# Optimization experiments

Measured on AMD Instinct MI355X. Metric: run time of the kernel, lower is better.

## Reference

```python
import jax, jax.numpy as jnp
import numpy as np

N_GROUP = 8
TOPK_GROUP = 4
TOP_K = 8
ROUTED_SCALING_FACTOR = 2.5


def setup_inputs() -> dict:
    key = jax.random.key(0)
    ks = jax.random.split(key, 6)
    T, H, I, E = 256, 1024, 512, 32
    x = jax.random.normal(ks[0], (T, H), dtype=jnp.float32)
    gate_w = jax.random.normal(ks[1], (H, E), dtype=jnp.float32) * 0.05
    e_score_bias = jax.random.normal(ks[2], (E,), dtype=jnp.float32) * 0.05
    Wg = jax.random.normal(ks[3], (E, H, I), dtype=jnp.float32) * 0.02
    Wu = jax.random.normal(ks[4], (E, H, I), dtype=jnp.float32) * 0.02
    Wd = jax.random.normal(ks[5], (E, I, H), dtype=jnp.float32) * 0.02
    return {"x": x, "gate_w": gate_w, "e_score_bias": e_score_bias,
            "Wg": Wg, "Wu": Wu, "Wd": Wd}


def _route_ds3(x, gate_w, e_score_bias):
    # DeepSeek-V3 group-limited top-k routing (routing_ds3 in source).
    T = x.shape[0]
    E = gate_w.shape[1]
    logits = x @ gate_w                      # [T, E]
    scores = jax.nn.sigmoid(logits)
    scores_for_choice = scores + e_score_bias[None, :]
    gsz = E // N_GROUP
    grouped = scores_for_choice.reshape(T, N_GROUP, gsz)
    # group score = sum of top-2 expert scores in group
    group_scores = jnp.sum(jax.lax.top_k(grouped, 2)[0], axis=-1)     # [T, n_group]
    _, group_idx = jax.lax.top_k(group_scores, TOPK_GROUP)            # [T, topk_group]
    rows = jnp.arange(T)[:, None]
    group_mask = jnp.zeros((T, N_GROUP), scores.dtype).at[rows, group_idx].set(1.0)
    score_mask = jnp.repeat(group_mask, gsz, axis=-1)                 # [T, E]
    masked = jnp.where(score_mask > 0, scores_for_choice, 0.0)
    _, topk_idx = jax.lax.top_k(masked, TOP_K)                        # [T, k]
    topk_w = jnp.take_along_axis(scores, topk_idx, axis=1)            # gather raw scores
    topk_w = topk_w / (jnp.sum(topk_w, axis=-1, keepdims=True) + 1e-20)
    topk_w = topk_w * ROUTED_SCALING_FACTOR
    return topk_idx, topk_w


def reference(x, gate_w, e_score_bias, Wg, Wu, Wd):
    T = x.shape[0]
    E = gate_w.shape[1]
    topk_idx, topk_w = _route_ds3(x, gate_w, e_score_bias)
    # dense [T, E] routing-weight matrix (topk indices are unique per row)
    rows = jnp.arange(T)[:, None]
    rw = jnp.zeros((T, E), x.dtype).at[rows, topk_idx].set(topk_w)
    # expert gated MLP (silu), combined with routing weights
    g = jnp.einsum('th,ehi->tei', x, Wg)      # [T, E, I]
    u = jnp.einsum('th,ehi->tei', x, Wu)
    a = jax.nn.silu(g) * u
    y = jnp.einsum('tei,eih->teh', a, Wd)     # [T, E, H]
    out = jnp.einsum('te,teh->th', rw, y)     # weighted combine
    return out
```

## Files before the change

kernel.cpp:

```cpp
#include <hip/hip_runtime.h>
#include <cstdint>
#include <cmath>

constexpr int TT   = 256;
constexpr int HD   = 1024;
constexpr int IDIM = 512;
constexpr int NE   = 32;
constexpr int NGRP = 8;
constexpr int TKG  = 4;
constexpr int TOPK = 8;
constexpr float RSCALE = 2.5f;

constexpr int NSX  = HD / 32;
constexpr int NSA  = IDIM / 32;
constexpr int SLAB = 16 * 64 * 8;

typedef float    f32x4 __attribute__((ext_vector_type(4)));
typedef _Float16 half8 __attribute__((ext_vector_type(8)));

constexpr size_t WS_CNT = 0;
constexpr size_t WS_TOK = 256;
constexpr size_t WS_WL  = WS_TOK + (size_t)NE * TT * 4;
constexpr size_t WS_XE  = WS_WL  + (size_t)NE * TT * 4;
constexpr size_t WS_A   = WS_XE  + (size_t)NE * NSX * SLAB * 2;

#define GLOAD16(GP, LP) __builtin_amdgcn_global_load_lds(                      \
    (const __attribute__((address_space(1))) unsigned int*)(GP),               \
    (__attribute__((address_space(3))) unsigned int*)(LP), 16, 0, 0)

__global__ __launch_bounds__(256) void k_route(
    const float* __restrict__ x, const float* __restrict__ gw,
    const float* __restrict__ bias, int* __restrict__ cnt,
    int* __restrict__ tok, float* __restrict__ wl)
{
    int t = blockIdx.x;
    int tid = threadIdx.x;
    int e2 = (tid & 15) * 2;
    int c  = tid >> 4;
    const float* xr = x + (size_t)t * HD;

    float a0 = 0.f, a1 = 0.f;
    int h0 = c * (HD / 16);
#pragma unroll 8
    for (int h = h0; h < h0 + HD / 16; ++h) {
        float xv = xr[h];
        float2 wv = *(const float2*)&gw[(size_t)h * NE + e2];
        a0 += xv * wv.x;
        a1 += xv * wv.y;
    }

    __shared__ float part[16][NE];
    part[c][e2]     = a0;
    part[c][e2 + 1] = a1;
    __syncthreads();

    __shared__ float sc[NE], sfc[NE];
    if (tid < NE) {
        float s = 0.f;
#pragma unroll
        for (int cc = 0; cc < 16; ++cc) s += part[cc][tid];
        float sig = 1.f / (1.f + expf(-s));
        sc[tid]  = sig;
        sfc[tid] = sig + bias[tid];
    }
    __syncthreads();

    if (tid == 0) {
        float gs[NGRP];
        for (int g = 0; g < NGRP; ++g) {
            float m1 = -3.0e38f, m2 = -3.0e38f;
            for (int j = 0; j < 4; ++j) {
                float v = sfc[4 * g + j];
                if (v > m1) { m2 = m1; m1 = v; } else if (v > m2) m2 = v;
            }
            gs[g] = m1 + m2;
        }
        bool gsel[NGRP];
        for (int g = 0; g < NGRP; ++g) gsel[g] = false;
        for (int r = 0; r < TKG; ++r) {
            int bi = -1; float bv = -3.0e38f;
            for (int g = 0; g < NGRP; ++g)
                if (!gsel[g] && gs[g] > bv) { bv = gs[g]; bi = g; }
            gsel[bi] = true;
        }
        float masked[NE];
        for (int i = 0; i < NE; ++i) masked[i] = gsel[i >> 2] ? sfc[i] : 0.0f;
        int   idx[TOPK]; float wv[TOPK]; float wsum = 0.f;
        for (int r = 0; r < TOPK; ++r) {
            int bi = -1; float bv = -3.0e38f;
            for (int i = 0; i < NE; ++i)
                if (masked[i] > bv) { bv = masked[i]; bi = i; }
            masked[bi] = -3.0e38f;
            idx[r] = bi; wv[r] = sc[bi]; wsum += wv[r];
        }
        float inv = RSCALE / (wsum + 1e-20f);
        for (int r = 0; r < TOPK; ++r) {
            int ee = idx[r];
            int pos = atomicAdd(&cnt[ee], 1);
            tok[(size_t)ee * TT + pos] = t;
            wl [(size_t)ee * TT + pos] = wv[r] * inv;
        }
    }
}

__global__ __launch_bounds__(256) void k_pack(
    const float* __restrict__ x, const int* __restrict__ cnt,
    const int* __restrict__ tok, _Float16* __restrict__ Xe)
{
    int bid  = blockIdx.x;
    int xcd  = bid & 7;
    int slot = bid >> 3;
    int e    = xcd * 4 + (slot & 3);
    int s    = slot >> 2;
    int n_e = cnt[e];
    if (n_e == 0) return;
    int tid = threadIdx.x, w = tid >> 6, lane = tid & 63;
    int m16 = lane & 15, q = lane >> 4;
    _Float16* base = Xe + ((size_t)e * NSX + s) * SLAB;
#pragma unroll
    for (int k = 0; k < 4; ++k) {
        int mt = w + k * 4;
        int slot2 = mt * 16 + m16;
        if (slot2 >= n_e) slot2 = n_e - 1;
        int t = tok[e * TT + slot2];
        const float* src = x + (size_t)t * HD + s * 32 + q * 8;
        f32x4 v0 = *(const f32x4*)src;
        f32x4 v1 = *(const f32x4*)(src + 4);
        half8 h;
        h[0] = (_Float16)v0.x; h[1] = (_Float16)v0.y; h[2] = (_Float16)v0.z; h[3] = (_Float16)v0.w;
        h[4] = (_Float16)v1.x; h[5] = (_Float16)v1.y; h[6] = (_Float16)v1.z; h[7] = (_Float16)v1.w;
        *(half8*)(base + ((size_t)mt * 64 + lane) * 8) = h;
    }
}

__global__ __launch_bounds__(128) void k_gateup(
    const _Float16* __restrict__ Xe, const float* __restrict__ Wg,
    const float* __restrict__ Wu, const int* __restrict__ cnt,
    _Float16* __restrict__ A)
{
    int bid  = blockIdx.x;
    int xcd  = bid & 7;
    int slot = bid >> 3;
    int e    = xcd * 4 + (slot & 3);
    int rest = slot >> 2;
    int ttile = rest & 1;
    int ig    = rest >> 1;
    int n_e = cnt[e];
    if (ttile * 128 >= n_e) return;
    int mtbase = ttile * 8;
    int i0 = ig * 32;
    int tid  = threadIdx.x;
    int w    = tid >> 6;
    int lane = tid & 63;
    int m16 = lane & 15, q = lane >> 4;
    int wcol = w * 16 + m16;

    __shared__ __align__(16) float LG[2][32][32];
    __shared__ __align__(16) float LU[2][32][32];

    const _Float16* abase = Xe + (size_t)e * NSX * SLAB + ((size_t)mtbase * 64 + lane) * 8;
    const float* gw0 = Wg + (size_t)e * HD * IDIM + i0;
    const float* uw0 = Wu + (size_t)e * HD * IDIM + i0;

    f32x4 accG[8], accU[8];
#pragma unroll
    for (int mt = 0; mt < 8; ++mt) {
        accG[mt] = (f32x4){0.f, 0.f, 0.f, 0.f};
        accU[mt] = (f32x4){0.f, 0.f, 0.f, 0.f};
    }

    half8 af0[8], af1[8];

#define GU_STAGE(B, KS)                                                        \
    { _Pragma("unroll")                                                        \
      for (int ci = 0; ci < 2; ++ci) {                                         \
        int c    = w * 2 + ci;                                                 \
        int row  = c * 8 + (lane >> 3);                                        \
        int csrc = ((lane & 7) << 2) ^ ((c & 1) << 4);                         \
        const float* gs = gw0 + ((size_t)(KS) * 32 + row) * IDIM + csrc;       \
        const float* us = uw0 + ((size_t)(KS) * 32 + row) * IDIM + csrc;       \
        GLOAD16(gs, &LG[B][c * 8][0]);                                         \
        GLOAD16(us, &LU[B][c * 8][0]);                                         \
      } }

#define GU_LOADA(KS, AF)                                                       \
    { const _Float16* a_ = abase + (size_t)(KS) * SLAB;                        \
      _Pragma("unroll")                                                        \
      for (int mt_ = 0; mt_ < 8; ++mt_) AF[mt_] = *(const half8*)(a_ + mt_ * 512); }

#define GU_COMPUTE(B, AF)                                                      \
    { int lc = wcol ^ ((q & 1) << 4);                                          \
      half8 bg, bu;                                                            \
      _Pragma("unroll")                                                        \
      for (int j_ = 0; j_ < 8; ++j_) {                                         \
        bg[j_] = (_Float16)LG[B][q * 8 + j_][lc];                              \
        bu[j_] = (_Float16)LU[B][q * 8 + j_][lc];                              \
      }                                                                        \
      _Pragma("unroll")                                                        \
      for (int mt_ = 0; mt_ < 8; ++mt_) {                                      \
        accG[mt_] = __builtin_amdgcn_mfma_f32_16x16x32_f16(AF[mt_], bg, accG[mt_], 0, 0, 0); \
        accU[mt_] = __builtin_amdgcn_mfma_f32_16x16x32_f16(AF[mt_], bu, accU[mt_], 0, 0, 0); \
      } }

    constexpr int NK = HD / 32;
    GU_STAGE(0, 0)
    GU_LOADA(0, af0)
    __syncthreads();

    for (int ks = 0; ks < NK; ks += 2) {
        GU_STAGE(1, ks + 1)
        GU_LOADA(ks + 1, af1)
        GU_COMPUTE(0, af0)
        __syncthreads();
        if (ks + 2 < NK) { GU_STAGE(0, ks + 2) GU_LOADA(ks + 2, af0) }
        GU_COMPUTE(1, af1)
        __syncthreads();
    }
#undef GU_STAGE
#undef GU_LOADA
#undef GU_COMPUTE

    int iyw = ig * 2 + w;
    _Float16* aout = A + ((size_t)e * NSA + (iyw >> 1)) * SLAB;
    int cj   = m16 & 7;
    int lsub = ((iyw * 2 + (m16 >> 3)) & 3) * 16;
#pragma unroll
    for (int mt = 0; mt < 8; ++mt) {
#pragma unroll
        for (int r = 0; r < 4; ++r) {
            float g = accG[mt][r], u = accU[mt][r];
            float a = (g / (1.f + expf(-g))) * u;
            int lp = (q * 4 + r) + lsub;
            aout[((size_t)(mtbase + mt) * 64 + lp) * 8 + cj] = (_Float16)a;
        }
    }
}

__global__ __launch_bounds__(128) void k_down(
    const _Float16* __restrict__ A, const float* __restrict__ Wd,
    const int* __restrict__ cnt, const int* __restrict__ tok,
    const float* __restrict__ wl, float* __restrict__ outf)
{
    int bid  = blockIdx.x;
    int xcd  = bid & 7;
    int slot = bid >> 3;
    int e    = xcd * 4 + (slot & 3);
    int rest = slot >> 2;
    int ttile = rest & 1;
    int hg    = rest >> 1;
    int n_e = cnt[e];
    if (ttile * 128 >= n_e) return;
    int mtbase = ttile * 8;
    int h0 = hg * 32;
    int tid  = threadIdx.x;
    int w    = tid >> 6;
    int lane = tid & 63;
    int m16 = lane & 15, q = lane >> 4;
    int wcol = w * 16 + m16;

    __shared__ __align__(16) float LD[2][32][32];

    const _Float16* abase = A + (size_t)e * NSA * SLAB + ((size_t)mtbase * 64 + lane) * 8;
    const float* dw0 = Wd + (size_t)e * IDIM * HD + h0;

    f32x4 acc[8];
#pragma unroll
    for (int mt = 0; mt < 8; ++mt) acc[mt] = (f32x4){0.f, 0.f, 0.f, 0.f};

    half8 af0[8], af1[8];

#define DN_STAGE(B, KS)                                                        \
    { _Pragma("unroll")                                                        \
      for (int ci = 0; ci < 2; ++ci) {                                         \
        int c    = w * 2 + ci;                                                 \
        int row  = c * 8 + (lane >> 3);                                        \
        int csrc = ((lane & 7) << 2) ^ ((c & 1) << 4);                         \
        const float* ds = dw0 + ((size_t)(KS) * 32 + row) * HD + csrc;         \
        GLOAD16(ds, &LD[B][c * 8][0]);                                         \
      } }

#define DN_LOADA(KS, AF)                                                       \
    { const _Float16* a_ = abase + (size_t)(KS) * SLAB;                        \
      _Pragma("unroll")                                                        \
      for (int mt_ = 0; mt_ < 8; ++mt_) AF[mt_] = *(const half8*)(a_ + mt_ * 512); }

#define DN_COMPUTE(B, AF)                                                      \
    { int lc = wcol ^ ((q & 1) << 4);                                          \
      half8 bd;                                                                \
      _Pragma("unroll")                                                        \
      for (int j_ = 0; j_ < 8; ++j_) bd[j_] = (_Float16)LD[B][q * 8 + j_][lc]; \
      _Pragma("unroll")                                                        \
      for (int mt_ = 0; mt_ < 8; ++mt_)                                        \
        acc[mt_] = __builtin_amdgcn_mfma_f32_16x16x32_f16(AF[mt_], bd, acc[mt_], 0, 0, 0); }

    constexpr int NK = IDIM / 32;
    DN_STAGE(0, 0)
    DN_LOADA(0, af0)
    __syncthreads();

    for (int ks = 0; ks < NK; ks += 2) {
        DN_STAGE(1, ks + 1)
        DN_LOADA(ks + 1, af1)
        DN_COMPUTE(0, af0)
        __syncthreads();
        if (ks + 2 < NK) { DN_STAGE(0, ks + 2) DN_LOADA(ks + 2, af0) }
        DN_COMPUTE(1, af1)
        __syncthreads();
    }
#undef DN_STAGE
#undef DN_LOADA
#undef DN_COMPUTE

    int col = h0 + w * 16 + m16;
#pragma unroll
    for (int mt = 0; mt < 8; ++mt) {
#pragma unroll
        for (int r = 0; r < 4; ++r) {
            int slot2 = ttile * 128 + mt * 16 + q * 4 + r;
            if (slot2 < n_e) {
                int t   = tok[(size_t)e * TT + slot2];
                float wt = wl[(size_t)e * TT + slot2];
                atomicAdd(&outf[(size_t)t * HD + col], wt * acc[mt][r]);
            }
        }
    }
}

extern "C" void kernel_launch(void* const* d_in, const int* in_sizes, int n_in,
                              void* d_out, int out_size, void* d_ws, size_t ws_size,
                              hipStream_t stream) {
    const float* x    = (const float*)d_in[0];
    const float* gw   = (const float*)d_in[1];
    const float* bias = (const float*)d_in[2];
    const float* Wg   = (const float*)d_in[3];
    const float* Wu   = (const float*)d_in[4];
    const float* Wd   = (const float*)d_in[5];
    float* out = (float*)d_out;

    char* ws = (char*)d_ws;
    int*      cnt = (int*)(ws + WS_CNT);
    int*      tok = (int*)(ws + WS_TOK);
    float*    wl  = (float*)(ws + WS_WL);
    _Float16* Xe  = (_Float16*)(ws + WS_XE);
    _Float16* A   = (_Float16*)(ws + WS_A);

    hipMemsetAsync(ws, 0, 256, stream);
    hipMemsetAsync(out, 0, (size_t)TT * HD * 4, stream);

    k_route<<<TT, 256, 0, stream>>>(x, gw, bias, cnt, tok, wl);
    k_pack<<<NE * NSX, 256, 0, stream>>>(x, cnt, tok, Xe);
    k_gateup<<<NE * 2 * (IDIM / 32), 128, 0, stream>>>(Xe, Wg, Wu, cnt, A);
    k_down<<<NE * 2 * (HD / 32), 128, 0, stream>>>(A, Wd, cnt, tok, wl, out);
}
```

Before: 290.1 us.

## Deepen gate-up and down GEMM pipelines with six-stage LDS ring and vmcnt waits

Replaces the double-buffered LDS staging in the gate/up and down expert GEMMs with a six-slot ring that prefetches weights four k-steps ahead and A fragments two steps ahead. A single barrier per k-step is guarded by explicit s_waitcnt vmcnt counts instead of full __syncthreads. The aim is to hide global memory latency on the weight streams. It raises LDS and register use (launch bounds now say one block per CU), and the hand-counted vmcnt values must match the compiler's issued load order or results will be corrupted.

```diff
diff --git a/kernel.cpp b/kernel.cpp
--- a/kernel.cpp
+++ b/kernel.cpp
@@ -27,6 +27,8 @@
 #define GLOAD16(GP, LP) __builtin_amdgcn_global_load_lds(                      \
     (const __attribute__((address_space(1))) unsigned int*)(GP),               \
     (__attribute__((address_space(3))) unsigned int*)(LP), 16, 0, 0)
+
+#define WAITVM(N) asm volatile("s_waitcnt vmcnt(" #N ")" ::: "memory")
 
 __global__ __launch_bounds__(256) void k_route(
     const float* __restrict__ x, const float* __restrict__ gw,
@@ -133,7 +135,7 @@
     }
 }
 
-__global__ __launch_bounds__(128) void k_gateup(
+__global__ __launch_bounds__(128, 1) void k_gateup(
     const _Float16* __restrict__ Xe, const float* __restrict__ Wg,
     const float* __restrict__ Wu, const int* __restrict__ cnt,
     _Float16* __restrict__ A)
@@ -155,8 +157,8 @@
     int m16 = lane & 15, q = lane >> 4;
     int wcol = w * 16 + m16;
 
-    __shared__ __align__(16) float LG[2][32][32];
-    __shared__ __align__(16) float LU[2][32][32];
+    __shared__ __align__(16) float LG[6][32][32];
+    __shared__ __align__(16) float LU[6][32][32];
 
     const _Float16* abase = Xe + (size_t)e * NSX * SLAB + ((size_t)mtbase * 64 + lane) * 8;
     const float* gw0 = Wg + (size_t)e * HD * IDIM + i0;
@@ -169,7 +171,7 @@
         accU[mt] = (f32x4){0.f, 0.f, 0.f, 0.f};
     }
 
-    half8 af0[8], af1[8];
+    half8 af[3][8];
 
 #define GU_STAGE(B, KS)                                                        \
     { _Pragma("unroll")                                                        \
@@ -203,18 +205,22 @@
       } }
 
     constexpr int NK = HD / 32;
-    GU_STAGE(0, 0)
-    GU_LOADA(0, af0)
-    __syncthreads();
-
-    for (int ks = 0; ks < NK; ks += 2) {
-        GU_STAGE(1, ks + 1)
-        GU_LOADA(ks + 1, af1)
-        GU_COMPUTE(0, af0)
-        __syncthreads();
-        if (ks + 2 < NK) { GU_STAGE(0, ks + 2) GU_LOADA(ks + 2, af0) }
-        GU_COMPUTE(1, af1)
-        __syncthreads();
+    GU_STAGE(0, 0) GU_STAGE(1, 1) GU_STAGE(2, 2) GU_STAGE(3, 3)
+    GU_LOADA(0, af[0]) GU_LOADA(1, af[1])
+
+#pragma unroll
+    for (int ks = 0; ks < NK; ++ks) {
+        if (ks + 4 < NK) GU_STAGE((ks + 4) % 6, ks + 4)
+        if (ks + 2 < NK) GU_LOADA(ks + 2, af[(ks + 2) % 3])
+        if      (ks == 0)      { WAITVM(20); }
+        else if (ks + 5 <= NK) { WAITVM(24); }
+        else if (ks + 4 == NK) { WAITVM(20); }
+        else if (ks + 3 == NK) { WAITVM(16); }
+        else if (ks + 2 == NK) { WAITVM(8);  }
+        else                   { WAITVM(0);  }
+        __builtin_amdgcn_s_barrier();
+        __builtin_amdgcn_sched_barrier(0);
+        GU_COMPUTE(ks % 6, af[ks % 3])
     }
 #undef GU_STAGE
 #undef GU_LOADA
@@ -236,7 +242,7 @@
     }
 }
 
-__global__ __launch_bounds__(128) void k_down(
+__global__ __launch_bounds__(128, 1) void k_down(
     const _Float16* __restrict__ A, const float* __restrict__ Wd,
     const int* __restrict__ cnt, const int* __restrict__ tok,
     const float* __restrict__ wl, float* __restrict__ outf)
@@ -258,7 +264,7 @@
     int m16 = lane & 15, q = lane >> 4;
     int wcol = w * 16 + m16;
 
-    __shared__ __align__(16) float LD[2][32][32];
+    __shared__ __align__(16) float LD[6][32][32];
 
     const _Float16* abase = A + (size_t)e * NSA * SLAB + ((size_t)mtbase * 64 + lane) * 8;
     const float* dw0 = Wd + (size_t)e * IDIM * HD + h0;
@@ -267,7 +273,7 @@
 #pragma unroll
     for (int mt = 0; mt < 8; ++mt) acc[mt] = (f32x4){0.f, 0.f, 0.f, 0.f};
 
-    half8 af0[8], af1[8];
+    half8 af[3][8];
 
 #define DN_STAGE(B, KS)                                                        \
     { _Pragma("unroll")                                                        \
@@ -294,18 +300,22 @@
         acc[mt_] = __builtin_amdgcn_mfma_f32_16x16x32_f16(AF[mt_], bd, acc[mt_], 0, 0, 0); }
 
     constexpr int NK = IDIM / 32;
-    DN_STAGE(0, 0)
-    DN_LOADA(0, af0)
-    __syncthreads();
-
-    for (int ks = 0; ks < NK; ks += 2) {
-        DN_STAGE(1, ks + 1)
-        DN_LOADA(ks + 1, af1)
-        DN_COMPUTE(0, af0)
-        __syncthreads();
-        if (ks + 2 < NK) { DN_STAGE(0, ks + 2) DN_LOADA(ks + 2, af0) }
-        DN_COMPUTE(1, af1)
-        __syncthreads();
+    DN_STAGE(0, 0) DN_STAGE(1, 1) DN_STAGE(2, 2) DN_STAGE(3, 3)
+    DN_LOADA(0, af[0]) DN_LOADA(1, af[1])
+
+#pragma unroll
+    for (int ks = 0; ks < NK; ++ks) {
+        if (ks + 4 < NK) DN_STAGE((ks + 4) % 6, ks + 4)
+        if (ks + 2 < NK) DN_LOADA(ks + 2, af[(ks + 2) % 3])
+        if      (ks == 0)      { WAITVM(18); }
+        else if (ks + 5 <= NK) { WAITVM(20); }
+        else if (ks + 4 == NK) { WAITVM(18); }
+        else if (ks + 3 == NK) { WAITVM(16); }
+        else if (ks + 2 == NK) { WAITVM(8);  }
+        else                   { WAITVM(0);  }
+        __builtin_amdgcn_s_barrier();
+        __builtin_amdgcn_sched_barrier(0);
+        DN_COMPUTE(ks % 6, af[ks % 3])
     }
 #undef DN_STAGE
 #undef DN_LOADA
```

Result: faster. 276.4 us (-4.7%).
